# Kernel optimization log

Hardware: AMD Instinct MI355X
Metric: run time of the kernel (lower is better)

Reference implementation:

```python
import jax, jax.numpy as jnp
import numpy as np

N_NODES = 100000


def gcn_conv(x, W, b, src, dst, num_nodes):
    # PyG GCNConv: add self-loops, symmetric deg^-1/2 normalization,
    # linear transform, scatter-add aggregation at dst, then bias.
    loop = jnp.arange(num_nodes, dtype=src.dtype)
    row = jnp.concatenate([src, loop])  # message sources
    col = jnp.concatenate([dst, loop])  # message destinations
    deg = jax.ops.segment_sum(jnp.ones_like(col, dtype=x.dtype), col,
                              num_segments=num_nodes)
    dinv = jnp.where(deg > 0, jax.lax.rsqrt(deg), 0.0)
    norm = dinv[row] * dinv[col]  # [E+N]
    h = x @ W  # [N, out]
    msg = h[row] * norm[:, None]  # gather + scale, [E+N, out]
    out = jax.ops.segment_sum(msg, col, num_segments=num_nodes)  # scatter-add
    return out + b


def setup_inputs() -> dict:
    key = jax.random.key(0)
    k1, k2, k3, k4, k5, k6 = jax.random.split(key, 6)
    dim_in, dim_h = 256, 128
    E = 1600000
    x = jax.random.normal(k1, (N_NODES, dim_in), dtype=jnp.float32)
    edge_index = jax.random.randint(k2, (2, E), 0, N_NODES, dtype=jnp.int64)
    # Glorot-style init for GCNConv weights
    W1 = jax.random.normal(k3, (dim_in, dim_h), dtype=jnp.float32) * (1.0 / np.sqrt(dim_in))
    b1 = jnp.zeros((dim_h,), dtype=jnp.float32)
    W2 = jax.random.normal(k4, (dim_h, 1), dtype=jnp.float32) * (1.0 / np.sqrt(dim_h))
    b2 = jnp.zeros((1,), dtype=jnp.float32)
    return {"x": x, "edge_index": edge_index, "W1": W1, "b1": b1, "W2": W2, "b2": b2}


def reference(x, edge_index, W1, b1, W2, b2):
    src, dst = edge_index[0], edge_index[1]
    h = gcn_conv(x, W1, b1, src, dst, N_NODES)
    h = jax.nn.relu(h)
    h = gcn_conv(h, W2, b2, src, dst, N_NODES)
    return jax.nn.sigmoid(h)  # [N, 1]
```

## Files before the change

kernel.cpp:

```cpp
#include <hip/hip_runtime.h>
#include <math.h>

#define NN 100000
#define DIN 256
#define DH 128
#define GEMM_NB 1563
#define BSHIFT 9
#define BNODES 512
#define NB_BUCKET 196
#define BCAP 12288
#define PA_EDGES 8192

using short8  = __attribute__((ext_vector_type(8))) short;
using float4v = __attribute__((ext_vector_type(4))) float;

static __device__ __forceinline__ unsigned short f2bf(float f) {
    unsigned u = __float_as_uint(f);
    unsigned r = u + 0x7fffu + ((u >> 16) & 1u);
    return (unsigned short)(r >> 16);
}
static __device__ __forceinline__ float bf_lo(unsigned u) { return __uint_as_float(u << 16); }
static __device__ __forceinline__ float bf_hi(unsigned u) { return __uint_as_float(u & 0xffff0000u); }

__global__ __launch_bounds__(256) void k_prepW(const float* __restrict__ W1,
                                               unsigned short* __restrict__ W1p) {
    int t = blockIdx.x * 256 + threadIdx.x;
    int lane = t & 63;
    int ks   = (t >> 6) & 7;
    int nt   = (t >> 9) & 1;
    int wv   = (t >> 10) & 3;
    int n = wv * 32 + nt * 16 + (lane & 15);
    int kbase = ks * 32 + (lane >> 4) * 8;
    short8 v;
#pragma unroll
    for (int j = 0; j < 8; ++j) v[j] = (short)f2bf(W1[(kbase + j) * DH + n]);
    *(short8*)&W1p[(long long)t * 8] = v;
}

__global__ __launch_bounds__(256) void k_gemm(const float* __restrict__ x,
                                              const unsigned short* __restrict__ W1p,
                                              unsigned short* __restrict__ hs) {
    __shared__ unsigned short aL[64 * 32 * 8];
    const int tid  = threadIdx.x;
    const int wave = tid >> 6;
    const int lane = tid & 63;
    const int quad = lane >> 4;
    const int m16  = lane & 15;
    const int row0 = blockIdx.x * 64;

    short8 bfr[2][8];
#pragma unroll
    for (int nt = 0; nt < 2; ++nt)
#pragma unroll
        for (int ks = 0; ks < 8; ++ks)
            bfr[nt][ks] = ((const short8*)W1p)[((wave * 2 + nt) * 8 + ks) * 64 + lane];

#pragma unroll
    for (int it = 0; it < 8; ++it) {
        int id  = it * 256 + tid;
        int row = id >> 5;
        int kb  = id & 31;
        int gr  = row0 + row;
        float4 f0, f1;
        if (gr < NN) {
            const float* xp = &x[(long long)gr * DIN + kb * 8];
            f0 = *(const float4*)xp;
            f1 = *(const float4*)(xp + 4);
        } else {
            f0 = make_float4(0.f, 0.f, 0.f, 0.f);
            f1 = f0;
        }
        short8 v;
        v[0] = (short)f2bf(f0.x); v[1] = (short)f2bf(f0.y);
        v[2] = (short)f2bf(f0.z); v[3] = (short)f2bf(f0.w);
        v[4] = (short)f2bf(f1.x); v[5] = (short)f2bf(f1.y);
        v[6] = (short)f2bf(f1.z); v[7] = (short)f2bf(f1.w);
        int chunk = row * 32 + (kb ^ (row & 31));
        *(short8*)&aL[chunk * 8] = v;
    }
    __syncthreads();

    float4v acc[4][2];
#pragma unroll
    for (int mt = 0; mt < 4; ++mt)
#pragma unroll
        for (int nt = 0; nt < 2; ++nt)
            acc[mt][nt] = (float4v)(0.0f);

#pragma unroll
    for (int mt = 0; mt < 4; ++mt) {
        int row = mt * 16 + m16;
#pragma unroll
        for (int ks = 0; ks < 8; ++ks) {
            int kb = ks * 4 + quad;
            int chunk = row * 32 + (kb ^ (row & 31));
            short8 a = *(const short8*)&aL[chunk * 8];
            acc[mt][0] = __builtin_amdgcn_mfma_f32_16x16x32_bf16(a, bfr[0][ks], acc[mt][0], 0, 0, 0);
            acc[mt][1] = __builtin_amdgcn_mfma_f32_16x16x32_bf16(a, bfr[1][ks], acc[mt][1], 0, 0, 0);
        }
    }

    const int n0 = wave * 32;
#pragma unroll
    for (int mt = 0; mt < 4; ++mt) {
#pragma unroll
        for (int r = 0; r < 4; ++r) {
            int row = row0 + mt * 16 + quad * 4 + r;
            if (row < NN) {
#pragma unroll
                for (int nt = 0; nt < 2; ++nt)
                    hs[(long long)row * DH + n0 + nt * 16 + m16] = f2bf(acc[mt][nt][r]);
            }
        }
    }
}

__global__ __launch_bounds__(512) void k_partA(const int* __restrict__ src,
                                               const int* __restrict__ dst, int E,
                                               int* __restrict__ bucketFill,
                                               int2* __restrict__ bucketArr) {
    __shared__ int aCnt[NB_BUCKET];
    __shared__ int aBase[NB_BUCKET];
    const int tid = threadIdx.x;
    for (int i = tid; i < NB_BUCKET; i += 512) aCnt[i] = 0;
    __syncthreads();
    const int e0   = blockIdx.x * PA_EDGES;
    const int eend = min(e0 + PA_EDGES, E);
    for (int e = e0 + tid; e < eend; e += 512)
        atomicAdd(&aCnt[dst[e] >> BSHIFT], 1);
    __syncthreads();
    for (int i = tid; i < NB_BUCKET; i += 512) {
        int c = aCnt[i];
        aBase[i] = c ? atomicAdd(&bucketFill[i], c) : 0;
        aCnt[i] = 0;
    }
    __syncthreads();
    for (int e = e0 + tid; e < eend; e += 512) {
        int d = dst[e];
        int b = d >> BSHIFT;
        int r = atomicAdd(&aCnt[b], 1);
        bucketArr[(long long)b * BCAP + aBase[b] + r] = make_int2(src[e], d);
    }
}

__global__ __launch_bounds__(512) void k_partB(const int* __restrict__ bucketFill,
                                               const int2* __restrict__ bucketArr,
                                               int* __restrict__ cnt,
                                               int* __restrict__ excl,
                                               float* __restrict__ dinv,
                                               int* __restrict__ eidx) {
    __shared__ int h[BNODES];
    __shared__ int hex[BNODES];
    __shared__ int st[256];
    const int tid   = threadIdx.x;
    const int b     = blockIdx.x;
    const int nbase = b << BSHIFT;
    const int len   = bucketFill[b];
    const long long abase = (long long)b * BCAP;

    if (tid < 256) st[tid] = (tid < b) ? bucketFill[tid] : 0;
    __syncthreads();
    for (int off = 128; off > 0; off >>= 1) {
        if (tid < off) st[tid] += st[tid + off];
        __syncthreads();
    }
    const int gbase = st[0];
    __syncthreads();

    for (int i = tid; i < BNODES; i += 512) h[i] = 0;
    __syncthreads();
    for (int k = tid; k < len; k += 512)
        atomicAdd(&h[bucketArr[abase + k].y - nbase], 1);
    __syncthreads();

    int a0 = 0, a1 = 0;
    if (tid < 256) {
        a0 = h[2 * tid]; a1 = h[2 * tid + 1];
        st[tid] = a0 + a1;
    }
    __syncthreads();
    for (int off = 1; off < 256; off <<= 1) {
        int val = (tid < 256 && tid >= off) ? st[tid - off] : 0;
        __syncthreads();
        if (tid < 256) st[tid] += val;
        __syncthreads();
    }
    if (tid < 256) {
        int prev = (tid > 0) ? st[tid - 1] : 0;
        hex[2 * tid]     = prev;
        hex[2 * tid + 1] = prev + a0;
    }
    __syncthreads();

    for (int i = tid; i < BNODES; i += 512) {
        int n = nbase + i;
        if (n < NN) {
            int c = h[i];
            cnt[n]  = c;
            excl[n] = gbase + hex[i];
            dinv[n] = rsqrtf(1.0f + (float)c);
        }
    }
    for (int i = tid; i < BNODES; i += 512) h[i] = 0;
    __syncthreads();

    for (int k = tid; k < len; k += 512) {
        int2 p = bucketArr[abase + k];
        int li = p.y - nbase;
        int r = atomicAdd(&h[li], 1);
        eidx[gbase + hex[li] + r] = p.x;
    }
}

__global__ __launch_bounds__(256) void k_agg1l2(const int* __restrict__ eidx,
                                                const int* __restrict__ excl,
                                                const int* __restrict__ cnt,
                                                const unsigned* __restrict__ hs2,
                                                const float* __restrict__ dinv,
                                                const float* __restrict__ b1,
                                                const float* __restrict__ W2,
                                                float* __restrict__ zs) {
    int w = (blockIdx.x * 256 + threadIdx.x) >> 6;
    if (w >= NN) return;
    int lane = threadIdx.x & 63;
    int offs = excl[w];
    int c = cnt[w];

    float dw = dinv[w];
    unsigned u = hs2[(long long)w * 64 + lane];
    float ax = dw * bf_lo(u);
    float ay = dw * bf_hi(u);

    int j = 0;
    for (; j + 7 < c; j += 8) {
        int s[8]; float es[8]; unsigned uu[8];
#pragma unroll
        for (int q = 0; q < 8; ++q) s[q] = eidx[offs + j + q];
#pragma unroll
        for (int q = 0; q < 8; ++q) es[q] = dinv[s[q]];
#pragma unroll
        for (int q = 0; q < 8; ++q) uu[q] = hs2[(long long)s[q] * 64 + lane];
#pragma unroll
        for (int q = 0; q < 8; ++q) {
            ax = fmaf(es[q], bf_lo(uu[q]), ax);
            ay = fmaf(es[q], bf_hi(uu[q]), ay);
        }
    }
    for (; j + 1 < c; j += 2) {
        int s0 = eidx[offs + j], s1 = eidx[offs + j + 1];
        float e0 = dinv[s0], e1 = dinv[s1];
        unsigned u0 = hs2[(long long)s0 * 64 + lane];
        unsigned u1 = hs2[(long long)s1 * 64 + lane];
        ax = fmaf(e0, bf_lo(u0), ax); ay = fmaf(e0, bf_hi(u0), ay);
        ax = fmaf(e1, bf_lo(u1), ax); ay = fmaf(e1, bf_hi(u1), ay);
    }
    if (j < c) {
        int s0 = eidx[offs + j];
        float e0 = dinv[s0];
        unsigned u0 = hs2[(long long)s0 * 64 + lane];
        ax = fmaf(e0, bf_lo(u0), ax); ay = fmaf(e0, bf_hi(u0), ay);
    }

    float2 bb = ((const float2*)b1)[lane];
    float2 ww = ((const float2*)W2)[lane];
    float r0 = fmaxf(fmaf(dw, ax, bb.x), 0.0f);
    float r1 = fmaxf(fmaf(dw, ay, bb.y), 0.0f);
    float v = r0 * ww.x + r1 * ww.y;
#pragma unroll
    for (int off = 32; off > 0; off >>= 1) v += __shfl_down(v, off);
    if (lane == 0) zs[w] = v * dw;
}

__global__ void k_agg2_final(const int* __restrict__ eidx,
                             const int* __restrict__ excl,
                             const int* __restrict__ cnt,
                             const float* __restrict__ zs,
                             const float* __restrict__ dinv,
                             const float* __restrict__ b2,
                             float* __restrict__ out) {
    int i = blockIdx.x * 256 + threadIdx.x;
    if (i >= NN) return;
    int offs = excl[i];
    int c = cnt[i];
    float v = zs[i];
    int j = 0;
    for (; j + 3 < c; j += 4) {
        int s0 = eidx[offs + j + 0];
        int s1 = eidx[offs + j + 1];
        int s2 = eidx[offs + j + 2];
        int s3 = eidx[offs + j + 3];
        v += zs[s0] + zs[s1] + zs[s2] + zs[s3];
    }
    for (; j < c; ++j) v += zs[eidx[offs + j]];
    float z = fmaf(dinv[i], v, b2[0]);
    out[i] = 1.0f / (1.0f + __expf(-z));
}

extern "C" void kernel_launch(void* const* d_in, const int* in_sizes, int n_in,
                              void* d_out, int out_size, void* d_ws, size_t ws_size,
                              hipStream_t stream) {
    const float* x  = (const float*)d_in[0];
    const int*   ei = (const int*)d_in[1];
    const float* W1 = (const float*)d_in[2];
    const float* b1 = (const float*)d_in[3];
    const float* W2 = (const float*)d_in[4];
    const float* b2 = (const float*)d_in[5];
    float* out = (float*)d_out;

    const int E = in_sizes[1] / 2;
    const int* src = ei;
    const int* dst = ei + E;

    int* wsi = (int*)d_ws;
    float* dinv       = (float*)wsi;
    int*   cnt        = wsi + NN;
    int*   excl       = cnt + NN;
    float* zs         = (float*)(excl + NN);
    int*   bucketFill = (int*)(zs + NN);
    unsigned short* W1p = (unsigned short*)(bucketFill + 256);
    int*   eidx       = (int*)(W1p + 32768);
    int2*  bucketArr  = (int2*)(eidx + E);
    unsigned short* hs = (unsigned short*)(bucketArr + (long long)NB_BUCKET * BCAP);

    const int nb_nodes = (NN + 255) / 256;
    const int pa_nb = (E + PA_EDGES - 1) / PA_EDGES;

    hipMemsetAsync(bucketFill, 0, NB_BUCKET * sizeof(int), stream);

    k_prepW<<<128, 256, 0, stream>>>(W1, W1p);
    k_partA<<<pa_nb, 512, 0, stream>>>(src, dst, E, bucketFill, bucketArr);
    k_partB<<<NB_BUCKET, 512, 0, stream>>>(bucketFill, bucketArr, cnt, excl, dinv, eidx);
    k_gemm<<<GEMM_NB, 256, 0, stream>>>(x, W1p, hs);

    k_agg1l2<<<(NN * 64 + 255) / 256, 256, 0, stream>>>(eidx, excl, cnt,
                                                        (const unsigned*)hs, dinv, b1, W2, zs);

    k_agg2_final<<<nb_nodes, 256, 0, stream>>>(eidx, excl, cnt, zs, dinv, b2, out);
}
```

Before: 300.7 us.

## Fuse weight prep into edge partition, pack bucket entries, deepen gather unroll

Merges the W1 bf16 packing kernel into the edge-partition kernel as extra blocks, removing one launch. The partition now stages src/dst in shared memory so dst is read once, uses smaller chunks with 256 threads, and packs each bucket entry into one 32-bit word (local dst in the high bits, src in the low 17 bits) instead of an int2. That halves bucket array traffic in both partition passes. The first aggregation kernel unrolls its gather to 16 edges to keep more loads in flight, at the cost of more registers.

```diff
diff --git a/kernel.cpp b/kernel.cpp
--- a/kernel.cpp
+++ b/kernel.cpp
@@ -9,7 +9,8 @@
 #define BNODES 512
 #define NB_BUCKET 196
 #define BCAP 12288
-#define PA_EDGES 8192
+#define PA_EDGES 4096
+#define PREPW_NB 128
 
 using short8  = __attribute__((ext_vector_type(8))) short;
 using float4v = __attribute__((ext_vector_type(4))) float;
@@ -22,19 +23,126 @@
 static __device__ __forceinline__ float bf_lo(unsigned u) { return __uint_as_float(u << 16); }
 static __device__ __forceinline__ float bf_hi(unsigned u) { return __uint_as_float(u & 0xffff0000u); }
 
-__global__ __launch_bounds__(256) void k_prepW(const float* __restrict__ W1,
-                                               unsigned short* __restrict__ W1p) {
-    int t = blockIdx.x * 256 + threadIdx.x;
-    int lane = t & 63;
-    int ks   = (t >> 6) & 7;
-    int nt   = (t >> 9) & 1;
-    int wv   = (t >> 10) & 3;
-    int n = wv * 32 + nt * 16 + (lane & 15);
-    int kbase = ks * 32 + (lane >> 4) * 8;
-    short8 v;
-#pragma unroll
-    for (int j = 0; j < 8; ++j) v[j] = (short)f2bf(W1[(kbase + j) * DH + n]);
-    *(short8*)&W1p[(long long)t * 8] = v;
+__global__ __launch_bounds__(256) void k_partA_prepW(const int* __restrict__ src,
+                                                     const int* __restrict__ dst, int E,
+                                                     int* __restrict__ bucketFill,
+                                                     unsigned* __restrict__ bkArr,
+                                                     int pa_nb,
+                                                     const float* __restrict__ W1,
+                                                     unsigned short* __restrict__ W1p) {
+    if ((int)blockIdx.x >= pa_nb) {
+        int t = ((int)blockIdx.x - pa_nb) * 256 + threadIdx.x;
+        int lane = t & 63;
+        int ks   = (t >> 6) & 7;
+        int nt   = (t >> 9) & 1;
+        int wv   = (t >> 10) & 3;
+        int n = wv * 32 + nt * 16 + (lane & 15);
+        int kbase = ks * 32 + (lane >> 4) * 8;
+        short8 v;
+#pragma unroll
+        for (int j = 0; j < 8; ++j) v[j] = (short)f2bf(W1[(kbase + j) * DH + n]);
+        *(short8*)&W1p[(long long)t * 8] = v;
+        return;
+    }
+    __shared__ int aCnt[NB_BUCKET];
+    __shared__ int aBase[NB_BUCKET];
+    __shared__ int ds[PA_EDGES];
+    __shared__ int ss[PA_EDGES];
+    const int tid = threadIdx.x;
+    for (int i = tid; i < NB_BUCKET; i += 256) aCnt[i] = 0;
+    __syncthreads();
+    const int e0   = (int)blockIdx.x * PA_EDGES;
+    const int eend = min(e0 + PA_EDGES, E);
+    const int n    = eend - e0;
+    for (int i = tid; i < n; i += 256) {
+        int d = dst[e0 + i];
+        ds[i] = d;
+        ss[i] = src[e0 + i];
+        atomicAdd(&aCnt[d >> BSHIFT], 1);
+    }
+    __syncthreads();
+    for (int i = tid; i < NB_BUCKET; i += 256) {
+        int c = aCnt[i];
+        aBase[i] = c ? atomicAdd(&bucketFill[i], c) : 0;
+        aCnt[i] = 0;
+    }
+    __syncthreads();
+    for (int i = tid; i < n; i += 256) {
+        int d = ds[i];
+        int b = d >> BSHIFT;
+        int r = atomicAdd(&aCnt[b], 1);
+        bkArr[(long long)b * BCAP + aBase[b] + r] =
+            ((unsigned)(d & (BNODES - 1)) << 17) | (unsigned)ss[i];
+    }
+}
+
+__global__ __launch_bounds__(512) void k_partB(const int* __restrict__ bucketFill,
+                                               const unsigned* __restrict__ bkArr,
+                                               int* __restrict__ cnt,
+                                               int* __restrict__ excl,
+                                               float* __restrict__ dinv,
+                                               int* __restrict__ eidx) {
+    __shared__ int h[BNODES];
+    __shared__ int hex[BNODES];
+    __shared__ int st[256];
+    const int tid   = threadIdx.x;
+    const int b     = blockIdx.x;
+    const int nbase = b << BSHIFT;
+    const int len   = bucketFill[b];
+    const long long abase = (long long)b * BCAP;
+
+    if (tid < 256) st[tid] = (tid < b) ? bucketFill[tid] : 0;
+    __syncthreads();
+    for (int off = 128; off > 0; off >>= 1) {
+        if (tid < off) st[tid] += st[tid + off];
+        __syncthreads();
+    }
+    const int gbase = st[0];
+    __syncthreads();
+
+    for (int i = tid; i < BNODES; i += 512) h[i] = 0;
+    __syncthreads();
+    for (int k = tid; k < len; k += 512)
+        atomicAdd(&h[bkArr[abase + k] >> 17], 1);
+    __syncthreads();
+
+    int a0 = 0, a1 = 0;
+    if (tid < 256) {
+        a0 = h[2 * tid]; a1 = h[2 * tid + 1];
+        st[tid] = a0 + a1;
+    }
+    __syncthreads();
+    for (int off = 1; off < 256; off <<= 1) {
+        int val = (tid < 256 && tid >= off) ? st[tid - off] : 0;
+        __syncthreads();
+        if (tid < 256) st[tid] += val;
+        __syncthreads();
+    }
+    if (tid < 256) {
+        int prev = (tid > 0) ? st[tid - 1] : 0;
+        hex[2 * tid]     = prev;
+        hex[2 * tid + 1] = prev + a0;
+    }
+    __syncthreads();
+
+    for (int i = tid; i < BNODES; i += 512) {
+        int n = nbase + i;
+        if (n < NN) {
+            int c = h[i];
+            cnt[n]  = c;
+            excl[n] = gbase + hex[i];
+            dinv[n] = rsqrtf(1.0f + (float)c);
+        }
+    }
+    for (int i = tid; i < BNODES; i += 512) h[i] = 0;
+    __syncthreads();
+
+    for (int k = tid; k < len; k += 512) {
+        unsigned w = bkArr[abase + k];
+        int li = (int)(w >> 17);
+        int r = atomicAdd(&h[li], 1);
+        eidx[gbase + hex[li] + r] = (int)(w & 0x1FFFFu);
+    }
 }
 
 __global__ __launch_bounds__(256) void k_gemm(const float* __restrict__ x,
@@ -115,103 +223,6 @@
     }
 }
 
-__global__ __launch_bounds__(512) void k_partA(const int* __restrict__ src,
-                                               const int* __restrict__ dst, int E,
-                                               int* __restrict__ bucketFill,
-                                               int2* __restrict__ bucketArr) {
-    __shared__ int aCnt[NB_BUCKET];
-    __shared__ int aBase[NB_BUCKET];
-    const int tid = threadIdx.x;
-    for (int i = tid; i < NB_BUCKET; i += 512) aCnt[i] = 0;
-    __syncthreads();
-    const int e0   = blockIdx.x * PA_EDGES;
-    const int eend = min(e0 + PA_EDGES, E);
-    for (int e = e0 + tid; e < eend; e += 512)
-        atomicAdd(&aCnt[dst[e] >> BSHIFT], 1);
-    __syncthreads();
-    for (int i = tid; i < NB_BUCKET; i += 512) {
-        int c = aCnt[i];
-        aBase[i] = c ? atomicAdd(&bucketFill[i], c) : 0;
-        aCnt[i] = 0;
-    }
-    __syncthreads();
-    for (int e = e0 + tid; e < eend; e += 512) {
-        int d = dst[e];
-        int b = d >> BSHIFT;
-        int r = atomicAdd(&aCnt[b], 1);
-        bucketArr[(long long)b * BCAP + aBase[b] + r] = make_int2(src[e], d);
-    }
-}
-
-__global__ __launch_bounds__(512) void k_partB(const int* __restrict__ bucketFill,
-                                               const int2* __restrict__ bucketArr,
-                                               int* __restrict__ cnt,
-                                               int* __restrict__ excl,
-                                               float* __restrict__ dinv,
-                                               int* __restrict__ eidx) {
-    __shared__ int h[BNODES];
-    __shared__ int hex[BNODES];
-    __shared__ int st[256];
-    const int tid   = threadIdx.x;
-    const int b     = blockIdx.x;
-    const int nbase = b << BSHIFT;
-    const int len   = bucketFill[b];
-    const long long abase = (long long)b * BCAP;
-
-    if (tid < 256) st[tid] = (tid < b) ? bucketFill[tid] : 0;
-    __syncthreads();
-    for (int off = 128; off > 0; off >>= 1) {
-        if (tid < off) st[tid] += st[tid + off];
-        __syncthreads();
-    }
-    const int gbase = st[0];
-    __syncthreads();
-
-    for (int i = tid; i < BNODES; i += 512) h[i] = 0;
-    __syncthreads();
-    for (int k = tid; k < len; k += 512)
-        atomicAdd(&h[bucketArr[abase + k].y - nbase], 1);
-    __syncthreads();
-
-    int a0 = 0, a1 = 0;
-    if (tid < 256) {
-        a0 = h[2 * tid]; a1 = h[2 * tid + 1];
-        st[tid] = a0 + a1;
-    }
-    __syncthreads();
-    for (int off = 1; off < 256; off <<= 1) {
-        int val = (tid < 256 && tid >= off) ? st[tid - off] : 0;
-        __syncthreads();
-        if (tid < 256) st[tid] += val;
-        __syncthreads();
-    }
-    if (tid < 256) {
-        int prev = (tid > 0) ? st[tid - 1] : 0;
-        hex[2 * tid]     = prev;
-        hex[2 * tid + 1] = prev + a0;
-    }
-    __syncthreads();
-
-    for (int i = tid; i < BNODES; i += 512) {
-        int n = nbase + i;
-        if (n < NN) {
-            int c = h[i];
-            cnt[n]  = c;
-            excl[n] = gbase + hex[i];
-            dinv[n] = rsqrtf(1.0f + (float)c);
-        }
-    }
-    for (int i = tid; i < BNODES; i += 512) h[i] = 0;
-    __syncthreads();
-
-    for (int k = tid; k < len; k += 512) {
-        int2 p = bucketArr[abase + k];
-        int li = p.y - nbase;
-        int r = atomicAdd(&h[li], 1);
-        eidx[gbase + hex[li] + r] = p.x;
-    }
-}
-
 __global__ __launch_bounds__(256) void k_agg1l2(const int* __restrict__ eidx,
                                                 const int* __restrict__ excl,
                                                 const int* __restrict__ cnt,
@@ -232,7 +243,21 @@
     float ay = dw * bf_hi(u);
 
     int j = 0;
-    for (; j + 7 < c; j += 8) {
+    for (; j + 15 < c; j += 16) {
+        int s[16]; float es[16]; unsigned uu[16];
+#pragma unroll
+        for (int q = 0; q < 16; ++q) s[q] = eidx[offs + j + q];
+#pragma unroll
+        for (int q = 0; q < 16; ++q) es[q] = dinv[s[q]];
+#pragma unroll
+        for (int q = 0; q < 16; ++q) uu[q] = hs2[(long long)s[q] * 64 + lane];
+#pragma unroll
+        for (int q = 0; q < 16; ++q) {
+            ax = fmaf(es[q], bf_lo(uu[q]), ax);
+            ay = fmaf(es[q], bf_hi(uu[q]), ay);
+        }
+    }
+    if (j + 7 < c) {
         int s[8]; float es[8]; unsigned uu[8];
 #pragma unroll
         for (int q = 0; q < 8; ++q) s[q] = eidx[offs + j + q];
@@ -245,6 +270,7 @@
             ax = fmaf(es[q], bf_lo(uu[q]), ax);
             ay = fmaf(es[q], bf_hi(uu[q]), ay);
         }
+        j += 8;
     }
     for (; j + 1 < c; j += 2) {
         int s0 = eidx[offs + j], s1 = eidx[offs + j + 1];
@@ -319,17 +345,17 @@
     int*   bucketFill = (int*)(zs + NN);
     unsigned short* W1p = (unsigned short*)(bucketFill + 256);
     int*   eidx       = (int*)(W1p + 32768);
-    int2*  bucketArr  = (int2*)(eidx + E);
-    unsigned short* hs = (unsigned short*)(bucketArr + (long long)NB_BUCKET * BCAP);
+    unsigned* bkArr   = (unsigned*)(eidx + E);
+    unsigned short* hs = (unsigned short*)(bkArr + (long long)NB_BUCKET * BCAP);
 
     const int nb_nodes = (NN + 255) / 256;
     const int pa_nb = (E + PA_EDGES - 1) / PA_EDGES;
 
     hipMemsetAsync(bucketFill, 0, NB_BUCKET * sizeof(int), stream);
 
-    k_prepW<<<128, 256, 0, stream>>>(W1, W1p);
-    k_partA<<<pa_nb, 512, 0, stream>>>(src, dst, E, bucketFill, bucketArr);
-    k_partB<<<NB_BUCKET, 512, 0, stream>>>(bucketFill, bucketArr, cnt, excl, dinv, eidx);
+    k_partA_prepW<<<pa_nb + PREPW_NB, 256, 0, stream>>>(src, dst, E, bucketFill, bkArr,
+                                                        pa_nb, W1, W1p);
+    k_partB<<<NB_BUCKET, 512, 0, stream>>>(bucketFill, bkArr, cnt, excl, dinv, eidx);
     k_gemm<<<GEMM_NB, 256, 0, stream>>>(x, W1p, hs);
 
     k_agg1l2<<<(NN * 64 + 255) / 256, 256, 0, stream>>>(eidx, excl, cnt,
```

Measured after the change: 315.4 us. 4.9% more time.
